# Optimization experiments

Measured on AMD Instinct MI355X. Metric: run time of the kernel, lower is better.

## Reference

```python
import jax, jax.numpy as jnp
import numpy as np

EPS = 1e-7
NUM_NODES = 50000


def setup_inputs() -> dict:
    key = jax.random.key(0)
    k1, k2, k3 = jax.random.split(key, 3)
    n_nodes, n_edges, d = NUM_NODES, 800000, 64
    x = jax.random.normal(k1, (n_nodes, d), dtype=jnp.float32)
    edge_index = jax.random.randint(k2, (2, n_edges), 0, n_nodes, dtype=jnp.int64)
    W = jax.random.normal(k3, (d, d), dtype=jnp.float32) * (1.0 / np.sqrt(d))
    b = jnp.zeros((d,), dtype=jnp.float32)
    beta = jnp.ones((1,), dtype=jnp.float32)
    return {"x": x, "edge_index": edge_index, "W": W, "b": b, "beta": beta}


def _segment_softmax(logits, seg, num_segments):
    # numerically stable softmax over edges grouped by destination node, per channel
    m = jax.ops.segment_max(logits, seg, num_segments=num_segments)  # [N, d]
    m = jnp.where(jnp.isfinite(m), m, 0.0)  # empty segments -> -inf; neutralize
    e = jnp.exp(logits - m[seg])                                      # [E, d]
    denom = jax.ops.segment_sum(e, seg, num_segments=num_segments)    # [N, d]
    return e / (denom[seg] + 1e-16)


def reference(x, edge_index, W, b, beta):
    num_nodes, dim = x.shape
    dst = edge_index[0]
    src = edge_index[1]
    # gather + message encoder (ReLU) + eps
    edge_msg = jax.nn.relu(x[src]) + EPS                               # [E, d]
    # softmax_sg: softmax(beta * msg) per destination segment, beta is a stop-grad scalar
    alpha = _segment_softmax(beta[0] * edge_msg, dst, num_nodes)       # [E, d]
    h = edge_msg * alpha                                               # [E, d]
    # scatter-add aggregation to destination nodes
    agg = jax.ops.segment_sum(h, dst, num_segments=num_nodes)          # [N, d]
    # final dense linear (nn.Linear): agg @ W.T + b
    return agg @ W.T + b
```

## Files before the change

kernel.cpp:

```cpp
#include <hip/hip_runtime.h>
#include <hip/hip_fp16.h>

#define EPS 1e-7f

__global__ __launch_bounds__(512)
void binprep_kernel(const int* __restrict__ dst,
                    const int* __restrict__ src, int E, int cap,
                    const float* __restrict__ x,
                    const float* __restrict__ beta, int M,
                    int* __restrict__ ccur,
                    unsigned* __restrict__ packed,
                    unsigned* __restrict__ tp,
                    int binBlocks) {
    if ((int)blockIdx.x < binBlocks) {
        __shared__ int lc[256];
        __shared__ int lbase[256];
        int tid = threadIdx.x;
        if (tid < 256) lc[tid] = 0;
        __syncthreads();
        int e0 = blockIdx.x * 2048;
        int bb[4], rr[4];
        unsigned pk[4];
        #pragma unroll
        for (int i = 0; i < 4; ++i) {
            int e = e0 + i * 512 + tid;
            bb[i] = 0; rr[i] = 0; pk[i] = 0;
            if (e < E) {
                int d = dst[e];
                bb[i] = d >> 8;
                pk[i] = ((unsigned)(d & 255) << 16) | (unsigned)src[e];
                rr[i] = atomicAdd(&lc[bb[i]], 1);
            }
        }
        __syncthreads();
        if (tid < 256) {
            int c = lc[tid];
            if (c) lbase[tid] = tid * cap + atomicAdd(&ccur[tid], c);
        }
        __syncthreads();
        #pragma unroll
        for (int i = 0; i < 4; ++i) {
            int e = e0 + i * 512 + tid;
            if (e < E) packed[lbase[bb[i]] + rr[i]] = pk[i];
        }
    } else {
        int blk = blockIdx.x - binBlocks;
        int tid = threadIdx.x;
        const float bt = beta[0];
        #pragma unroll
        for (int p = 0; p < 4; ++p) {
            int i = blk * 8192 + p * 2048 + tid * 4;
            if (i < M) {
                float4 v = *(const float4*)&x[i];
                uint4 o;
                float m, ex;
                m = fmaxf(v.x, 0.f) + EPS; ex = __expf(bt * m);
                o.x = (unsigned)__half_as_ushort(__float2half_rn(ex)) |
                      ((unsigned)__half_as_ushort(__float2half_rn(m * ex)) << 16);
                m = fmaxf(v.y, 0.f) + EPS; ex = __expf(bt * m);
                o.y = (unsigned)__half_as_ushort(__float2half_rn(ex)) |
                      ((unsigned)__half_as_ushort(__float2half_rn(m * ex)) << 16);
                m = fmaxf(v.z, 0.f) + EPS; ex = __expf(bt * m);
                o.z = (unsigned)__half_as_ushort(__float2half_rn(ex)) |
                      ((unsigned)__half_as_ushort(__float2half_rn(m * ex)) << 16);
                m = fmaxf(v.w, 0.f) + EPS; ex = __expf(bt * m);
                o.w = (unsigned)__half_as_ushort(__float2half_rn(ex)) |
                      ((unsigned)__half_as_ushort(__float2half_rn(m * ex)) << 16);
                *(uint4*)&tp[i] = o;
            } else if (i < M + 64) {
                uint4 o; o.x = o.y = o.z = o.w = 0u;
                *(uint4*)&tp[i] = o;
            }
        }
    }
}

__global__ __launch_bounds__(512)
void fine_kernel(const unsigned* __restrict__ packed,
                 const int* __restrict__ ccur, int cap,
                 int2* __restrict__ nse,
                 unsigned short* __restrict__ sorted_src, int N) {
    __shared__ int lc[256];
    __shared__ int lcur[256];
    __shared__ int wsum[4];
    __shared__ unsigned stage_pk[6656];
    __shared__ unsigned short stage16[6656];
    int tid = threadIdx.x, b = blockIdx.x;
    int rs = b * cap;
    int len = ccur[b];
    if (tid < 256) lc[tid] = 0;
    __syncthreads();
    for (int i = tid; i < len; i += 512) {
        unsigned u = packed[rs + i];
        stage_pk[i] = u;
        atomicAdd(&lc[u >> 16], 1);
    }
    __syncthreads();
    if (tid < 256) {
        int lane = tid & 63, wid = tid >> 6;
        int incl = lc[tid];
        #pragma unroll
        for (int d = 1; d < 64; d <<= 1) {
            int t = __shfl_up(incl, d, 64);
            if (lane >= d) incl += t;
        }
        lcur[tid] = incl;
        if (lane == 63) wsum[wid] = incl;
    }
    __syncthreads();
    if (tid < 256) {
        int wid = tid >> 6;
        int base = 0;
        for (int w = 0; w < wid; ++w) base += wsum[w];
        int v = lc[tid];
        int excl = base + lcur[tid] - v;
        lcur[tid] = excl;
        int node = b * 256 + tid;
        if (node < N) nse[node] = make_int2(rs + excl, rs + excl + v);
    }
    __syncthreads();
    for (int i = tid; i < len; i += 512) {
        unsigned u = stage_pk[i];
        int pos = atomicAdd(&lcur[u >> 16], 1);
        stage16[pos] = (unsigned short)(u & 0xffffu);
    }
    __syncthreads();
    unsigned* dst32 = (unsigned*)&sorted_src[rs];
    int len2 = (len + 1) >> 1;
    for (int i = tid; i < len2; i += 512) {
        unsigned lo = stage16[2 * i];
        unsigned hi = (2 * i + 1 < len) ? (unsigned)stage16[2 * i + 1] : 0u;
        dst32[i] = lo | (hi << 16);
    }
}

__device__ __forceinline__ float f16lo(unsigned w) {
    return __half2float(__ushort_as_half((unsigned short)(w & 0xffffu)));
}
__device__ __forceinline__ float f16hi(unsigned w) {
    return __half2float(__ushort_as_half((unsigned short)(w >> 16)));
}

__global__ __launch_bounds__(256)
void node_kernel(const unsigned* __restrict__ tp,
                 const int2* __restrict__ nse,
                 const unsigned short* __restrict__ ss,
                 float* __restrict__ agg, int N) {
    const int tid = threadIdx.x;
    const int wave = tid >> 6;
    const int lane = tid & 63;
    const int quarter = lane >> 4;
    const int l16 = lane & 15;
    const int qbase = quarter << 4;
    const int chb = l16 << 4;
    const int sent = N << 8;
    const unsigned char* tb = (const unsigned char*)tp;

    const int node = blockIdx.x * 16 + wave * 4 + quarter;
    int start = 0, cnt = 0;
    if (node < N) { int2 se = nse[node]; start = se.x; cnt = se.y - se.x; }

    float s1x = 0.f, s1y = 0.f, s1z = 0.f, s1w = 0.f;
    float s2x = 0.f, s2y = 0.f, s2z = 0.f, s2w = 0.f;

    for (int chunk = 0; chunk < cnt; chunk += 16) {
        int rem = cnt - chunk;
        if (rem > 16) rem = 16;
        int row = (l16 < rem) ? ((int)ss[start + chunk + l16] << 8) : sent;
        for (int k = 0; k < rem; k += 4) {
            int r0 = __shfl(row, qbase + k + 0, 64);
            int r1 = __shfl(row, qbase + k + 1, 64);
            int r2 = __shfl(row, qbase + k + 2, 64);
            int r3 = __shfl(row, qbase + k + 3, 64);
            uint4 u0 = *(const uint4*)(tb + (r0 + chb));
            uint4 u1 = *(const uint4*)(tb + (r1 + chb));
            uint4 u2 = *(const uint4*)(tb + (r2 + chb));
            uint4 u3 = *(const uint4*)(tb + (r3 + chb));
            #define ACC(u) \
                s1x += f16lo(u.x); s2x += f16hi(u.x); \
                s1y += f16lo(u.y); s2y += f16hi(u.y); \
                s1z += f16lo(u.z); s2z += f16hi(u.z); \
                s1w += f16lo(u.w); s2w += f16hi(u.w)
            ACC(u0); ACC(u1); ACC(u2); ACC(u3);
            #undef ACC
        }
    }
    if (node < N) {
        float4 g;
        g.x = __fdividef(s2x, s1x + 1e-16f);
        g.y = __fdividef(s2y, s1y + 1e-16f);
        g.z = __fdividef(s2z, s1z + 1e-16f);
        g.w = __fdividef(s2w, s1w + 1e-16f);
        *(float4*)&agg[((size_t)node << 6) + (l16 << 2)] = g;
    }
}

__global__ __launch_bounds__(256)
void linear_kernel(const float* __restrict__ agg,
                   const float* __restrict__ W,
                   const float* __restrict__ b,
                   float* __restrict__ out, int N) {
    __shared__ float WtS[64 * 65];
    __shared__ float aggS[256];
    int tid = threadIdx.x;
    #pragma unroll
    for (int idx = tid * 4; idx < 64 * 64; idx += 256 * 4) {
        float4 w4 = *(const float4*)&W[idx];
        int j = idx >> 6, c = idx & 63;
        WtS[(c + 0) * 65 + j] = w4.x;
        WtS[(c + 1) * 65 + j] = w4.y;
        WtS[(c + 2) * 65 + j] = w4.z;
        WtS[(c + 3) * 65 + j] = w4.w;
    }
    __syncthreads();
    const int wave = tid >> 6;
    const int lane = tid & 63;
    const float bias = b[lane];
    const int stride = gridDim.x * 4;
    float* as = &aggS[wave * 64];
    for (int node = blockIdx.x * 4 + wave; node < N; node += stride) {
        as[lane] = agg[(size_t)node * 64 + lane];
        float acc = bias;
        #pragma unroll
        for (int c = 0; c < 64; c += 4) {
            float4 a4 = *(const float4*)&as[c];
            acc = fmaf(a4.x, WtS[(c + 0) * 65 + lane], acc);
            acc = fmaf(a4.y, WtS[(c + 1) * 65 + lane], acc);
            acc = fmaf(a4.z, WtS[(c + 2) * 65 + lane], acc);
            acc = fmaf(a4.w, WtS[(c + 3) * 65 + lane], acc);
        }
        out[(size_t)node * 64 + lane] = acc;
    }
}

extern "C" void kernel_launch(void* const* d_in, const int* in_sizes, int n_in,
                              void* d_out, int out_size, void* d_ws, size_t ws_size,
                              hipStream_t stream) {
    const float* x    = (const float*)d_in[0];
    const int*   ei   = (const int*)d_in[1];
    const float* W    = (const float*)d_in[2];
    const float* b    = (const float*)d_in[3];
    const float* beta = (const float*)d_in[4];
    float* out = (float*)d_out;

    const int N = in_sizes[0] / 64;
    const int E = in_sizes[1] / 2;
    const int* dst = ei;
    const int* src = ei + E;
    const int NB = (N + 255) >> 8;
    const int M = N * 64;

    int cap = (E + NB - 1) / NB;
    cap = ((cap + cap / 2 + 256) + 255) & ~255;
    if (cap > 6656) cap = 6656;

    auto align = [](size_t v) { return (v + 255) & ~(size_t)255; };
    size_t off = 0;
    char* ws = (char*)d_ws;
    int2* nse   = (int2*)(ws + off);      off += align((size_t)N * 8);
    int* ccur   = (int*)(ws + off);       off += align((size_t)NB * 4);
    unsigned* packed = (unsigned*)(ws + off);
    off += align((size_t)NB * cap * 4);
    unsigned short* sorted_src = (unsigned short*)(ws + off);
    off += align((size_t)NB * cap * 2);
    unsigned* tp = (unsigned*)(ws + off); off += align(((size_t)N + 1) * 64 * 4);
    float* agg  = (float*)(ws + off);     off += align((size_t)M * 4);

    const int binBlocks  = (E + 2047) / 2048;
    const int prepBlocks = (M + 64 + 8191) / 8192;
    hipMemsetAsync(ccur, 0, (size_t)NB * 4, stream);
    binprep_kernel<<<binBlocks + prepBlocks, 512, 0, stream>>>(
        dst, src, E, cap, x, beta, M, ccur, packed, tp, binBlocks);
    fine_kernel<<<NB, 512, 0, stream>>>(packed, ccur, cap, nse, sorted_src, N);
    node_kernel<<<(N + 15) / 16, 256, 0, stream>>>(tp, nse, sorted_src, agg, N);

    int lin_blocks = (N + 3) / 4;
    if (lin_blocks > 2048) lin_blocks = 2048;
    linear_kernel<<<lin_blocks, 256, 0, stream>>>(agg, W, b, out, N);
}
```

Before: 133.6 us.

## Fuse fine sort, node aggregation and linear into one per-bin kernel

New measurement: 153.3 us. +14.8%, slower.

```diff
diff --git a/kernel.cpp b/kernel.cpp
--- a/kernel.cpp
+++ b/kernel.cpp
@@ -2,10 +2,12 @@
 #include <hip/hip_fp16.h>
 
 #define EPS 1e-7f
+#define CAP 2048
+#define NBK 784
 
 __global__ __launch_bounds__(512)
 void binprep_kernel(const int* __restrict__ dst,
-                    const int* __restrict__ src, int E, int cap,
+                    const int* __restrict__ src, int E, int NB,
                     const float* __restrict__ x,
                     const float* __restrict__ beta, int M,
                     int* __restrict__ ccur,
@@ -13,33 +15,33 @@
                     unsigned* __restrict__ tp,
                     int binBlocks) {
     if ((int)blockIdx.x < binBlocks) {
-        __shared__ int lc[256];
-        __shared__ int lbase[256];
+        __shared__ int lc[NBK];
+        __shared__ int lbase[NBK];
         int tid = threadIdx.x;
-        if (tid < 256) lc[tid] = 0;
+        for (int i = tid; i < NB; i += 512) lc[i] = 0;
         __syncthreads();
-        int e0 = blockIdx.x * 2048;
-        int bb[4], rr[4];
-        unsigned pk[4];
-        #pragma unroll
-        for (int i = 0; i < 4; ++i) {
+        int e0 = blockIdx.x * 8192;
+        int bb[16], rr[16];
+        unsigned pk[16];
+        #pragma unroll
+        for (int i = 0; i < 16; ++i) {
             int e = e0 + i * 512 + tid;
             bb[i] = 0; rr[i] = 0; pk[i] = 0;
             if (e < E) {
                 int d = dst[e];
-                bb[i] = d >> 8;
-                pk[i] = ((unsigned)(d & 255) << 16) | (unsigned)src[e];
+                bb[i] = d >> 6;
+                pk[i] = ((unsigned)(d & 63) << 16) | (unsigned)src[e];
                 rr[i] = atomicAdd(&lc[bb[i]], 1);
             }
         }
         __syncthreads();
-        if (tid < 256) {
-            int c = lc[tid];
-            if (c) lbase[tid] = tid * cap + atomicAdd(&ccur[tid], c);
+        for (int i = tid; i < NB; i += 512) {
+            int c = lc[i];
+            if (c) lbase[i] = i * CAP + atomicAdd(&ccur[i], c);
         }
         __syncthreads();
         #pragma unroll
-        for (int i = 0; i < 4; ++i) {
+        for (int i = 0; i < 16; ++i) {
             int e = e0 + i * 512 + tid;
             if (e < E) packed[lbase[bb[i]] + rr[i]] = pk[i];
         }
@@ -75,78 +77,73 @@
     }
 }
 
-__global__ __launch_bounds__(512)
-void fine_kernel(const unsigned* __restrict__ packed,
-                 const int* __restrict__ ccur, int cap,
-                 int2* __restrict__ nse,
-                 unsigned short* __restrict__ sorted_src, int N) {
-    __shared__ int lc[256];
-    __shared__ int lcur[256];
-    __shared__ int wsum[4];
-    __shared__ unsigned stage_pk[6656];
-    __shared__ unsigned short stage16[6656];
-    int tid = threadIdx.x, b = blockIdx.x;
-    int rs = b * cap;
+__device__ __forceinline__ float f16lo(unsigned w) {
+    return __half2float(__ushort_as_half((unsigned short)(w & 0xffffu)));
+}
+__device__ __forceinline__ float f16hi(unsigned w) {
+    return __half2float(__ushort_as_half((unsigned short)(w >> 16)));
+}
+
+__global__ __launch_bounds__(256)
+void mega_kernel(const unsigned* __restrict__ packed,
+                 const int* __restrict__ ccur,
+                 const unsigned* __restrict__ tp,
+                 const float* __restrict__ W,
+                 const float* __restrict__ bias,
+                 float* __restrict__ out, int N) {
+    __shared__ unsigned stage_pk[CAP];
+    __shared__ unsigned short stage16[CAP];
+    __shared__ float WtS[64 * 65];
+    __shared__ float aggS[64][64];
+    __shared__ int lc[64];
+    __shared__ int nstart[64];
+    __shared__ int lcur[64];
+
+    const int tid = threadIdx.x;
+    const int b = blockIdx.x;
+
+    #pragma unroll
+    for (int idx = tid * 4; idx < 64 * 64; idx += 256 * 4) {
+        float4 w4 = *(const float4*)&W[idx];
+        int j = idx >> 6, c = idx & 63;
+        WtS[(c + 0) * 65 + j] = w4.x;
+        WtS[(c + 1) * 65 + j] = w4.y;
+        WtS[(c + 2) * 65 + j] = w4.z;
+        WtS[(c + 3) * 65 + j] = w4.w;
+    }
+    if (tid < 64) lc[tid] = 0;
+    __syncthreads();
+
     int len = ccur[b];
-    if (tid < 256) lc[tid] = 0;
-    __syncthreads();
-    for (int i = tid; i < len; i += 512) {
+    if (len > CAP) len = CAP;
+    const int rs = b * CAP;
+    for (int i = tid; i < len; i += 256) {
         unsigned u = packed[rs + i];
         stage_pk[i] = u;
         atomicAdd(&lc[u >> 16], 1);
     }
     __syncthreads();
-    if (tid < 256) {
-        int lane = tid & 63, wid = tid >> 6;
-        int incl = lc[tid];
+
+    if (tid < 64) {
+        int v = lc[tid];
+        int incl = v;
         #pragma unroll
         for (int d = 1; d < 64; d <<= 1) {
             int t = __shfl_up(incl, d, 64);
-            if (lane >= d) incl += t;
-        }
-        lcur[tid] = incl;
-        if (lane == 63) wsum[wid] = incl;
-    }
-    __syncthreads();
-    if (tid < 256) {
-        int wid = tid >> 6;
-        int base = 0;
-        for (int w = 0; w < wid; ++w) base += wsum[w];
-        int v = lc[tid];
-        int excl = base + lcur[tid] - v;
-        lcur[tid] = excl;
-        int node = b * 256 + tid;
-        if (node < N) nse[node] = make_int2(rs + excl, rs + excl + v);
-    }
-    __syncthreads();
-    for (int i = tid; i < len; i += 512) {
+            if (tid >= d) incl += t;
+        }
+        nstart[tid] = incl - v;
+        lcur[tid] = incl - v;
+    }
+    __syncthreads();
+
+    for (int i = tid; i < len; i += 256) {
         unsigned u = stage_pk[i];
         int pos = atomicAdd(&lcur[u >> 16], 1);
         stage16[pos] = (unsigned short)(u & 0xffffu);
     }
     __syncthreads();
-    unsigned* dst32 = (unsigned*)&sorted_src[rs];
-    int len2 = (len + 1) >> 1;
-    for (int i = tid; i < len2; i += 512) {
-        unsigned lo = stage16[2 * i];
-        unsigned hi = (2 * i + 1 < len) ? (unsigned)stage16[2 * i + 1] : 0u;
-        dst32[i] = lo | (hi << 16);
-    }
-}
-
-__device__ __forceinline__ float f16lo(unsigned w) {
-    return __half2float(__ushort_as_half((unsigned short)(w & 0xffffu)));
-}
-__device__ __forceinline__ float f16hi(unsigned w) {
-    return __half2float(__ushort_as_half((unsigned short)(w >> 16)));
-}
-
-__global__ __launch_bounds__(256)
-void node_kernel(const unsigned* __restrict__ tp,
-                 const int2* __restrict__ nse,
-                 const unsigned short* __restrict__ ss,
-                 float* __restrict__ agg, int N) {
-    const int tid = threadIdx.x;
+
     const int wave = tid >> 6;
     const int lane = tid & 63;
     const int quarter = lane >> 4;
@@ -156,80 +153,60 @@
     const int sent = N << 8;
     const unsigned char* tb = (const unsigned char*)tp;
 
-    const int node = blockIdx.x * 16 + wave * 4 + quarter;
-    int start = 0, cnt = 0;
-    if (node < N) { int2 se = nse[node]; start = se.x; cnt = se.y - se.x; }
-
-    float s1x = 0.f, s1y = 0.f, s1z = 0.f, s1w = 0.f;
-    float s2x = 0.f, s2y = 0.f, s2z = 0.f, s2w = 0.f;
-
-    for (int chunk = 0; chunk < cnt; chunk += 16) {
-        int rem = cnt - chunk;
-        if (rem > 16) rem = 16;
-        int row = (l16 < rem) ? ((int)ss[start + chunk + l16] << 8) : sent;
-        for (int k = 0; k < rem; k += 4) {
-            int r0 = __shfl(row, qbase + k + 0, 64);
-            int r1 = __shfl(row, qbase + k + 1, 64);
-            int r2 = __shfl(row, qbase + k + 2, 64);
-            int r3 = __shfl(row, qbase + k + 3, 64);
-            uint4 u0 = *(const uint4*)(tb + (r0 + chb));
-            uint4 u1 = *(const uint4*)(tb + (r1 + chb));
-            uint4 u2 = *(const uint4*)(tb + (r2 + chb));
-            uint4 u3 = *(const uint4*)(tb + (r3 + chb));
-            #define ACC(u) \
-                s1x += f16lo(u.x); s2x += f16hi(u.x); \
-                s1y += f16lo(u.y); s2y += f16hi(u.y); \
-                s1z += f16lo(u.z); s2z += f16hi(u.z); \
-                s1w += f16lo(u.w); s2w += f16hi(u.w)
-            ACC(u0); ACC(u1); ACC(u2); ACC(u3);
-            #undef ACC
-        }
-    }
-    if (node < N) {
+    #pragma unroll
+    for (int sweep = 0; sweep < 4; ++sweep) {
+        const int ln = sweep * 16 + wave * 4 + quarter;
+        const int start = nstart[ln];
+        const int cnt = lc[ln];
+        float s1x = 0.f, s1y = 0.f, s1z = 0.f, s1w = 0.f;
+        float s2x = 0.f, s2y = 0.f, s2z = 0.f, s2w = 0.f;
+        for (int chunk = 0; chunk < cnt; chunk += 16) {
+            int rem = cnt - chunk;
+            if (rem > 16) rem = 16;
+            int row = (l16 < rem) ? ((int)stage16[start + chunk + l16] << 8)
+                                  : sent;
+            for (int k = 0; k < rem; k += 4) {
+                int r0 = __shfl(row, qbase + k + 0, 64);
+                int r1 = __shfl(row, qbase + k + 1, 64);
+                int r2 = __shfl(row, qbase + k + 2, 64);
+                int r3 = __shfl(row, qbase + k + 3, 64);
+                uint4 u0 = *(const uint4*)(tb + (r0 + chb));
+                uint4 u1 = *(const uint4*)(tb + (r1 + chb));
+                uint4 u2 = *(const uint4*)(tb + (r2 + chb));
+                uint4 u3 = *(const uint4*)(tb + (r3 + chb));
+                #define ACC(u) \
+                    s1x += f16lo(u.x); s2x += f16hi(u.x); \
+                    s1y += f16lo(u.y); s2y += f16hi(u.y); \
+                    s1z += f16lo(u.z); s2z += f16hi(u.z); \
+                    s1w += f16lo(u.w); s2w += f16hi(u.w)
+                ACC(u0); ACC(u1); ACC(u2); ACC(u3);
+                #undef ACC
+            }
+        }
         float4 g;
         g.x = __fdividef(s2x, s1x + 1e-16f);
         g.y = __fdividef(s2y, s1y + 1e-16f);
         g.z = __fdividef(s2z, s1z + 1e-16f);
         g.w = __fdividef(s2w, s1w + 1e-16f);
-        *(float4*)&agg[((size_t)node << 6) + (l16 << 2)] = g;
-    }
-}
-
-__global__ __launch_bounds__(256)
-void linear_kernel(const float* __restrict__ agg,
-                   const float* __restrict__ W,
-                   const float* __restrict__ b,
-                   float* __restrict__ out, int N) {
-    __shared__ float WtS[64 * 65];
-    __shared__ float aggS[256];
-    int tid = threadIdx.x;
-    #pragma unroll
-    for (int idx = tid * 4; idx < 64 * 64; idx += 256 * 4) {
-        float4 w4 = *(const float4*)&W[idx];
-        int j = idx >> 6, c = idx & 63;
-        WtS[(c + 0) * 65 + j] = w4.x;
-        WtS[(c + 1) * 65 + j] = w4.y;
-        WtS[(c + 2) * 65 + j] = w4.z;
-        WtS[(c + 3) * 65 + j] = w4.w;
-    }
-    __syncthreads();
-    const int wave = tid >> 6;
-    const int lane = tid & 63;
-    const float bias = b[lane];
-    const int stride = gridDim.x * 4;
-    float* as = &aggS[wave * 64];
-    for (int node = blockIdx.x * 4 + wave; node < N; node += stride) {
-        as[lane] = agg[(size_t)node * 64 + lane];
-        float acc = bias;
+        *(float4*)&aggS[ln][l16 << 2] = g;
+    }
+    __syncthreads();
+
+    const float bv = bias[lane];
+    const int nodeBase = b << 6;
+    for (int ln = wave; ln < 64; ln += 4) {
+        int node = nodeBase + ln;
+        if (node >= N) continue;
+        float acc = bv;
         #pragma unroll
         for (int c = 0; c < 64; c += 4) {
-            float4 a4 = *(const float4*)&as[c];
+            float4 a4 = *(const float4*)&aggS[ln][c];
             acc = fmaf(a4.x, WtS[(c + 0) * 65 + lane], acc);
             acc = fmaf(a4.y, WtS[(c + 1) * 65 + lane], acc);
             acc = fmaf(a4.z, WtS[(c + 2) * 65 + lane], acc);
             acc = fmaf(a4.w, WtS[(c + 3) * 65 + lane], acc);
         }
-        out[(size_t)node * 64 + lane] = acc;
+        out[((size_t)node << 6) + lane] = acc;
     }
 }
 
@@ -247,34 +224,21 @@
     const int E = in_sizes[1] / 2;
     const int* dst = ei;
     const int* src = ei + E;
-    const int NB = (N + 255) >> 8;
+    const int NB = (N + 63) >> 6;
     const int M = N * 64;
-
-    int cap = (E + NB - 1) / NB;
-    cap = ((cap + cap / 2 + 256) + 255) & ~255;
-    if (cap > 6656) cap = 6656;
 
     auto align = [](size_t v) { return (v + 255) & ~(size_t)255; };
     size_t off = 0;
     char* ws = (char*)d_ws;
-    int2* nse   = (int2*)(ws + off);      off += align((size_t)N * 8);
-    int* ccur   = (int*)(ws + off);       off += align((size_t)NB * 4);
+    int* ccur = (int*)(ws + off);         off += align((size_t)NB * 4);
     unsigned* packed = (unsigned*)(ws + off);
-    off += align((size_t)NB * cap * 4);
-    unsigned short* sorted_src = (unsigned short*)(ws + off);
-    off += align((size_t)NB * cap * 2);
+    off += align((size_t)NB * CAP * 4);
     unsigned* tp = (unsigned*)(ws + off); off += align(((size_t)N + 1) * 64 * 4);
-    float* agg  = (float*)(ws + off);     off += align((size_t)M * 4);
-
-    const int binBlocks  = (E + 2047) / 2048;
+
+    const int binBlocks  = (E + 8191) / 8192;
     const int prepBlocks = (M + 64 + 8191) / 8192;
     hipMemsetAsync(ccur, 0, (size_t)NB * 4, stream);
     binprep_kernel<<<binBlocks + prepBlocks, 512, 0, stream>>>(
-        dst, src, E, cap, x, beta, M, ccur, packed, tp, binBlocks);
-    fine_kernel<<<NB, 512, 0, stream>>>(packed, ccur, cap, nse, sorted_src, N);
-    node_kernel<<<(N + 15) / 16, 256, 0, stream>>>(tp, nse, sorted_src, agg, N);
-
-    int lin_blocks = (N + 3) / 4;
-    if (lin_blocks > 2048) lin_blocks = 2048;
-    linear_kernel<<<lin_blocks, 256, 0, stream>>>(agg, W, b, out, N);
-}
+        dst, src, E, NB, x, beta, M, ccur, packed, tp, binBlocks);
+    mega_kernel<<<NB, 256, 0, stream>>>(packed, ccur, tp, W, b, out, N);
+}
```

## Store fp16 messages only, compute exp in gather, use MFMA for linear layer

Applied to the files above, without the earlier changes.

Result: slower. 139.3 us (+4.3%).

```diff
diff --git a/kernel.cpp b/kernel.cpp
--- a/kernel.cpp
+++ b/kernel.cpp
@@ -2,15 +2,19 @@
 #include <hip/hip_fp16.h>
 
 #define EPS 1e-7f
+
+typedef _Float16 half8 __attribute__((ext_vector_type(8)));
+typedef float f32x4 __attribute__((ext_vector_type(4)));
 
 __global__ __launch_bounds__(512)
 void binprep_kernel(const int* __restrict__ dst,
                     const int* __restrict__ src, int E, int cap,
                     const float* __restrict__ x,
-                    const float* __restrict__ beta, int M,
+                    const float* __restrict__ W, int M,
                     int* __restrict__ ccur,
                     unsigned* __restrict__ packed,
-                    unsigned* __restrict__ tp,
+                    unsigned short* __restrict__ tm,
+                    unsigned short* __restrict__ Wh,
                     int binBlocks) {
     if ((int)blockIdx.x < binBlocks) {
         __shared__ int lc[256];
@@ -46,30 +50,28 @@
     } else {
         int blk = blockIdx.x - binBlocks;
         int tid = threadIdx.x;
-        const float bt = beta[0];
+        if (blk == 0) {
+            #pragma unroll
+            for (int j = 0; j < 8; ++j) {
+                int i = tid * 8 + j;
+                Wh[i] = __half_as_ushort(__float2half_rn(W[i]));
+            }
+        }
+        const unsigned short sent = __half_as_ushort(__float2half_rn(-32.f));
         #pragma unroll
         for (int p = 0; p < 4; ++p) {
             int i = blk * 8192 + p * 2048 + tid * 4;
             if (i < M) {
                 float4 v = *(const float4*)&x[i];
-                uint4 o;
-                float m, ex;
-                m = fmaxf(v.x, 0.f) + EPS; ex = __expf(bt * m);
-                o.x = (unsigned)__half_as_ushort(__float2half_rn(ex)) |
-                      ((unsigned)__half_as_ushort(__float2half_rn(m * ex)) << 16);
-                m = fmaxf(v.y, 0.f) + EPS; ex = __expf(bt * m);
-                o.y = (unsigned)__half_as_ushort(__float2half_rn(ex)) |
-                      ((unsigned)__half_as_ushort(__float2half_rn(m * ex)) << 16);
-                m = fmaxf(v.z, 0.f) + EPS; ex = __expf(bt * m);
-                o.z = (unsigned)__half_as_ushort(__float2half_rn(ex)) |
-                      ((unsigned)__half_as_ushort(__float2half_rn(m * ex)) << 16);
-                m = fmaxf(v.w, 0.f) + EPS; ex = __expf(bt * m);
-                o.w = (unsigned)__half_as_ushort(__float2half_rn(ex)) |
-                      ((unsigned)__half_as_ushort(__float2half_rn(m * ex)) << 16);
-                *(uint4*)&tp[i] = o;
+                ushort4 o;
+                o.x = __half_as_ushort(__float2half_rn(fmaxf(v.x, 0.f) + EPS));
+                o.y = __half_as_ushort(__float2half_rn(fmaxf(v.y, 0.f) + EPS));
+                o.z = __half_as_ushort(__float2half_rn(fmaxf(v.z, 0.f) + EPS));
+                o.w = __half_as_ushort(__float2half_rn(fmaxf(v.w, 0.f) + EPS));
+                *(ushort4*)&tm[i] = o;
             } else if (i < M + 64) {
-                uint4 o; o.x = o.y = o.z = o.w = 0u;
-                *(uint4*)&tp[i] = o;
+                ushort4 o; o.x = o.y = o.z = o.w = sent;
+                *(ushort4*)&tm[i] = o;
             }
         }
     }
@@ -134,29 +136,30 @@
     }
 }
 
-__device__ __forceinline__ float f16lo(unsigned w) {
+__device__ __forceinline__ float hlo(unsigned w) {
     return __half2float(__ushort_as_half((unsigned short)(w & 0xffffu)));
 }
-__device__ __forceinline__ float f16hi(unsigned w) {
+__device__ __forceinline__ float hhi(unsigned w) {
     return __half2float(__ushort_as_half((unsigned short)(w >> 16)));
 }
 
 __global__ __launch_bounds__(256)
-void node_kernel(const unsigned* __restrict__ tp,
-                 const int2* __restrict__ nse,
-                 const unsigned short* __restrict__ ss,
-                 float* __restrict__ agg, int N) {
+void gather_kernel(const unsigned short* __restrict__ tm,
+                   const int2* __restrict__ nse,
+                   const unsigned short* __restrict__ ss,
+                   const float* __restrict__ beta,
+                   unsigned short* __restrict__ agg16, int N) {
     const int tid = threadIdx.x;
-    const int wave = tid >> 6;
     const int lane = tid & 63;
     const int quarter = lane >> 4;
     const int l16 = lane & 15;
     const int qbase = quarter << 4;
-    const int chb = l16 << 4;
-    const int sent = N << 8;
-    const unsigned char* tb = (const unsigned char*)tp;
-
-    const int node = blockIdx.x * 16 + wave * 4 + quarter;
+    const int chb = l16 << 3;
+    const int sent = N << 7;
+    const unsigned char* tb = (const unsigned char*)tm;
+    const float c = beta[0] * 1.4426950408889634f;
+
+    const int node = blockIdx.x * 16 + (tid >> 6) * 4 + quarter;
     int start = 0, cnt = 0;
     if (node < N) { int2 se = nse[node]; start = se.x; cnt = se.y - se.x; }
 
@@ -166,70 +169,83 @@
     for (int chunk = 0; chunk < cnt; chunk += 16) {
         int rem = cnt - chunk;
         if (rem > 16) rem = 16;
-        int row = (l16 < rem) ? ((int)ss[start + chunk + l16] << 8) : sent;
-        for (int k = 0; k < rem; k += 4) {
+        int row = (l16 < rem) ? ((int)ss[start + chunk + l16] << 7) : sent;
+        #pragma unroll
+        for (int k = 0; k < 16; k += 4) {
             int r0 = __shfl(row, qbase + k + 0, 64);
             int r1 = __shfl(row, qbase + k + 1, 64);
             int r2 = __shfl(row, qbase + k + 2, 64);
             int r3 = __shfl(row, qbase + k + 3, 64);
-            uint4 u0 = *(const uint4*)(tb + (r0 + chb));
-            uint4 u1 = *(const uint4*)(tb + (r1 + chb));
-            uint4 u2 = *(const uint4*)(tb + (r2 + chb));
-            uint4 u3 = *(const uint4*)(tb + (r3 + chb));
-            #define ACC(u) \
-                s1x += f16lo(u.x); s2x += f16hi(u.x); \
-                s1y += f16lo(u.y); s2y += f16hi(u.y); \
-                s1z += f16lo(u.z); s2z += f16hi(u.z); \
-                s1w += f16lo(u.w); s2w += f16hi(u.w)
+            uint2 u0 = *(const uint2*)(tb + (r0 + chb));
+            uint2 u1 = *(const uint2*)(tb + (r1 + chb));
+            uint2 u2 = *(const uint2*)(tb + (r2 + chb));
+            uint2 u3 = *(const uint2*)(tb + (r3 + chb));
+            #define ACC(u) { \
+                float m0 = hlo(u.x), m1 = hhi(u.x); \
+                float m2 = hlo(u.y), m3 = hhi(u.y); \
+                float e0 = exp2f(m0 * c), e1 = exp2f(m1 * c); \
+                float e2 = exp2f(m2 * c), e3 = exp2f(m3 * c); \
+                s1x += e0; s2x = fmaf(m0, e0, s2x); \
+                s1y += e1; s2y = fmaf(m1, e1, s2y); \
+                s1z += e2; s2z = fmaf(m2, e2, s2z); \
+                s1w += e3; s2w = fmaf(m3, e3, s2w); }
             ACC(u0); ACC(u1); ACC(u2); ACC(u3);
             #undef ACC
         }
     }
     if (node < N) {
-        float4 g;
-        g.x = __fdividef(s2x, s1x + 1e-16f);
-        g.y = __fdividef(s2y, s1y + 1e-16f);
-        g.z = __fdividef(s2z, s1z + 1e-16f);
-        g.w = __fdividef(s2w, s1w + 1e-16f);
-        *(float4*)&agg[((size_t)node << 6) + (l16 << 2)] = g;
+        float gx = __fdividef(s2x, s1x + 1e-16f);
+        float gy = __fdividef(s2y, s1y + 1e-16f);
+        float gz = __fdividef(s2z, s1z + 1e-16f);
+        float gw = __fdividef(s2w, s1w + 1e-16f);
+        uint2 o;
+        o.x = (unsigned)__half_as_ushort(__float2half_rn(gx)) |
+              ((unsigned)__half_as_ushort(__float2half_rn(gy)) << 16);
+        o.y = (unsigned)__half_as_ushort(__float2half_rn(gz)) |
+              ((unsigned)__half_as_ushort(__float2half_rn(gw)) << 16);
+        *(uint2*)((unsigned char*)agg16 + ((size_t)node << 7) + chb) = o;
     }
 }
 
 __global__ __launch_bounds__(256)
-void linear_kernel(const float* __restrict__ agg,
-                   const float* __restrict__ W,
+void linear_kernel(const unsigned short* __restrict__ agg16,
+                   const unsigned short* __restrict__ Wh,
                    const float* __restrict__ b,
-                   float* __restrict__ out, int N) {
-    __shared__ float WtS[64 * 65];
-    __shared__ float aggS[256];
-    int tid = threadIdx.x;
-    #pragma unroll
-    for (int idx = tid * 4; idx < 64 * 64; idx += 256 * 4) {
-        float4 w4 = *(const float4*)&W[idx];
-        int j = idx >> 6, c = idx & 63;
-        WtS[(c + 0) * 65 + j] = w4.x;
-        WtS[(c + 1) * 65 + j] = w4.y;
-        WtS[(c + 2) * 65 + j] = w4.z;
-        WtS[(c + 3) * 65 + j] = w4.w;
-    }
-    __syncthreads();
+                   float* __restrict__ out, int N, int G) {
+    const int tid = threadIdx.x;
     const int wave = tid >> 6;
     const int lane = tid & 63;
-    const float bias = b[lane];
-    const int stride = gridDim.x * 4;
-    float* as = &aggS[wave * 64];
-    for (int node = blockIdx.x * 4 + wave; node < N; node += stride) {
-        as[lane] = agg[(size_t)node * 64 + lane];
-        float acc = bias;
-        #pragma unroll
-        for (int c = 0; c < 64; c += 4) {
-            float4 a4 = *(const float4*)&as[c];
-            acc = fmaf(a4.x, WtS[(c + 0) * 65 + lane], acc);
-            acc = fmaf(a4.y, WtS[(c + 1) * 65 + lane], acc);
-            acc = fmaf(a4.z, WtS[(c + 2) * 65 + lane], acc);
-            acc = fmaf(a4.w, WtS[(c + 3) * 65 + lane], acc);
-        }
-        out[(size_t)node * 64 + lane] = acc;
+    const int l16 = lane & 15;
+    const int quad = lane >> 4;
+    const int g = blockIdx.x * 4 + wave;
+    if (g >= G) return;
+
+    const unsigned char* ab = (const unsigned char*)agg16;
+    const unsigned char* wb = (const unsigned char*)Wh;
+
+    half8 a0 = *(const half8*)(ab + (((size_t)(g * 16 + l16)) << 7) + quad * 16);
+    half8 a1 = *(const half8*)(ab + (((size_t)(g * 16 + l16)) << 7) + 64 + quad * 16);
+
+    f32x4 acc[4];
+    float bias[4];
+    #pragma unroll
+    for (int t = 0; t < 4; ++t) {
+        const unsigned char* wr = wb + (((size_t)(16 * t + l16)) << 7) + quad * 16;
+        half8 b0 = *(const half8*)(wr);
+        half8 b1 = *(const half8*)(wr + 64);
+        acc[t] = (f32x4){0.f, 0.f, 0.f, 0.f};
+        acc[t] = __builtin_amdgcn_mfma_f32_16x16x32_f16(a0, b0, acc[t], 0, 0, 0);
+        acc[t] = __builtin_amdgcn_mfma_f32_16x16x32_f16(a1, b1, acc[t], 0, 0, 0);
+        bias[t] = b[16 * t + l16];
+    }
+    #pragma unroll
+    for (int t = 0; t < 4; ++t) {
+        #pragma unroll
+        for (int r = 0; r < 4; ++r) {
+            int node = g * 16 + quad * 4 + r;
+            if (node < N)
+                out[((size_t)node << 6) + 16 * t + l16] = acc[t][r] + bias[t];
+        }
     }
 }
 
@@ -249,6 +265,7 @@
     const int* src = ei + E;
     const int NB = (N + 255) >> 8;
     const int M = N * 64;
+    const int G = (N + 15) / 16;
 
     int cap = (E + NB - 1) / NB;
     cap = ((cap + cap / 2 + 256) + 255) & ~255;
@@ -257,24 +274,25 @@
     auto align = [](size_t v) { return (v + 255) & ~(size_t)255; };
     size_t off = 0;
     char* ws = (char*)d_ws;
-    int2* nse   = (int2*)(ws + off);      off += align((size_t)N * 8);
-    int* ccur   = (int*)(ws + off);       off += align((size_t)NB * 4);
+    int2* nse = (int2*)(ws + off);        off += align((size_t)N * 8);
+    int* ccur = (int*)(ws + off);         off += align((size_t)NB * 4);
     unsigned* packed = (unsigned*)(ws + off);
     off += align((size_t)NB * cap * 4);
     unsigned short* sorted_src = (unsigned short*)(ws + off);
     off += align((size_t)NB * cap * 2);
-    unsigned* tp = (unsigned*)(ws + off); off += align(((size_t)N + 1) * 64 * 4);
-    float* agg  = (float*)(ws + off);     off += align((size_t)M * 4);
+    unsigned short* tm = (unsigned short*)(ws + off);
+    off += align(((size_t)N + 1) * 64 * 2);
+    unsigned short* agg16 = (unsigned short*)(ws + off);
+    off += align((size_t)G * 16 * 64 * 2);
+    unsigned short* Wh = (unsigned short*)(ws + off);
+    off += align(64 * 64 * 2);
 
     const int binBlocks  = (E + 2047) / 2048;
     const int prepBlocks = (M + 64 + 8191) / 8192;
     hipMemsetAsync(ccur, 0, (size_t)NB * 4, stream);
     binprep_kernel<<<binBlocks + prepBlocks, 512, 0, stream>>>(
-        dst, src, E, cap, x, beta, M, ccur, packed, tp, binBlocks);
+        dst, src, E, cap, x, W, M, ccur, packed, tm, Wh, binBlocks);
     fine_kernel<<<NB, 512, 0, stream>>>(packed, ccur, cap, nse, sorted_src, N);
-    node_kernel<<<(N + 15) / 16, 256, 0, stream>>>(tp, nse, sorted_src, agg, N);
-
-    int lin_blocks = (N + 3) / 4;
-    if (lin_blocks > 2048) lin_blocks = 2048;
-    linear_kernel<<<lin_blocks, 256, 0, stream>>>(agg, W, b, out, N);
-}
+    gather_kernel<<<G, 256, 0, stream>>>(tm, nse, sorted_src, beta, agg16, N);
+    linear_kernel<<<(G + 3) / 4, 256, 0, stream>>>(agg16, Wh, b, out, N, G);
+}
```
